# Kernel tuning notes

Hardware: AMD Instinct MI355X
Metric: run time of the kernel (lower is better)

The kernel has to match this reference:

```python
import jax, jax.numpy as jnp
import numpy as np

D = 128      # n_hidden
NC = 4       # n_chan
DEPTH = 2
VD_DEPTH = 1
VD_ATTACH = 0
NV = 100000  # n_verts
PE_LEVELS = 6


def _mlp(x, Ws, bs):
    # MLP: Linear -> ReLU -> Linear -> ReLU -> Linear
    h = jax.nn.relu(x @ Ws[0] + bs[0])
    h = jax.nn.relu(h @ Ws[1] + bs[1])
    return h @ Ws[2] + bs[2]


def setup_inputs() -> dict:
    key = jax.random.key(0)
    ks = jax.random.split(key, 20)
    N, H, W = 2, 512, 512
    inp = {}
    inp["vert_idx_img"] = jax.random.randint(ks[0], (N, H, W, 3), 0, NV, dtype=jnp.int64) if jax.config.read("jax_enable_x64") else jax.random.randint(ks[0], (N, H, W, 3), 0, NV, dtype=jnp.int32)
    inp["bary_img"] = jax.random.uniform(ks[1], (N, H, W, 3), dtype=jnp.float32)
    inp["view_dir"] = jax.random.normal(ks[2], (N, H, W, 3), dtype=jnp.float32)
    # params
    s = D ** (-0.5)
    inp["emb_table"] = jax.random.normal(ks[3], (NV + 1, D), dtype=jnp.float32) * s
    k_lin = np.sqrt(2.0 / D).astype(np.float32)
    inp["vde_W"] = jax.random.normal(ks[4], (3 * PE_LEVELS, D), dtype=jnp.float32) * np.sqrt(2.0 / (3 * PE_LEVELS)).astype(np.float32)
    inp["vde_b"] = jnp.zeros((D,), jnp.float32)
    inp["vh_W"] = jax.random.normal(ks[5], (VD_DEPTH, 3, D, D), dtype=jnp.float32) * k_lin
    inp["vh_b"] = jnp.zeros((VD_DEPTH, 3, D), jnp.float32)
    inp["hid_W"] = jax.random.normal(ks[6], (DEPTH, 3, D, D), dtype=jnp.float32) * k_lin
    inp["hid_b"] = jnp.zeros((DEPTH, 3, D), jnp.float32)
    inp["head_W0"] = jax.random.normal(ks[7], (D, D), dtype=jnp.float32) * k_lin
    inp["head_b0"] = jnp.zeros((D,), jnp.float32)
    inp["head_W1"] = jax.random.normal(ks[8], (D, D), dtype=jnp.float32) * k_lin
    inp["head_b1"] = jnp.zeros((D,), jnp.float32)
    inp["head_W2"] = jax.random.normal(ks[9], (D, NC), dtype=jnp.float32) * k_lin
    inp["head_b2"] = jnp.zeros((NC,), jnp.float32)
    return inp


def reference(vert_idx_img, bary_img, view_dir, emb_table, vde_W, vde_b, vh_W, vh_b,
              hid_W, hid_b, head_W0, head_b0, head_W1, head_b1, head_W2, head_b2):
    # --- embedding gather with max_norm=1.0 renorm (torch nn.Embedding semantics)
    idx = vert_idx_img + 1                       # [N,H,W,3]
    e = emb_table[idx]                           # [N,H,W,3,D]
    nrm = jnp.linalg.norm(e, axis=-1, keepdims=True)
    e = e * jnp.where(nrm > 1.0, 1.0 / (nrm + 1e-7), 1.0)
    # --- barycentric weighted sum over the 3 face vertices
    v = jnp.sum(e * bary_img[..., None], axis=3)  # [N,H,W,D]
    # --- view-direction sin/cos positional encoding (proj_dims=6, val=0.9)
    ll = PE_LEVELS // 2
    exb = 2.0 * jnp.arange(ll, dtype=jnp.float32) / PE_LEVELS
    sigma = 2.0 * jnp.pi / jnp.power(0.9, exb)    # [3]
    pe = view_dir[..., None] * sigma              # [N,H,W,3,3]
    pe = jnp.concatenate([jnp.sin(pe), jnp.cos(pe)], axis=-1)  # [N,H,W,3,6]
    pe = pe.reshape(pe.shape[:-2] + (3 * PE_LEVELS,))           # [N,H,W,18]
    vh = pe @ vde_W + vde_b                       # [N,H,W,D]
    for i in range(vh_W.shape[0]):
        vh = jax.nn.relu(_mlp(vh, vh_W[i], vh_b[i]))
    # --- hidden MLP chain with view-dir modulation at viewdirs_attach
    h = v
    for i in range(hid_W.shape[0]):
        h = jax.nn.relu(_mlp(h, hid_W[i], hid_b[i]))
        if i == VD_ATTACH:
            h = h * vh
    # --- head MLP -> rgba
    rgb = _mlp(h, (head_W0, head_W1, head_W2), (head_b0, head_b1, head_b2))
    return rgb
```

## Files before the change

kernel.cpp:

```cpp
#include <hip/hip_runtime.h>

typedef unsigned int  u32;
typedef unsigned long long u64;
typedef unsigned short u16;
typedef __attribute__((ext_vector_type(8))) _Float16 h8;
typedef __attribute__((ext_vector_type(2))) _Float16 h2;
typedef __attribute__((ext_vector_type(4))) float    f4;

#define RS    136
#define PRS   40
#define PIXB  128
#define WOFF  5120
#define FULLT 16384
#define MFMA16 __builtin_amdgcn_mfma_f32_16x16x32_f16

__device__ __forceinline__ u16 f2h(float f) {
  _Float16 h = (_Float16)f;
  return __builtin_bit_cast(u16, h);
}
__device__ __forceinline__ u32 pkrtz(float a, float b) {
  return __builtin_bit_cast(u32, __builtin_amdgcn_cvt_pkrtz(a, b));
}
__device__ __forceinline__ u32 pkmul(u32 a, u32 b) {
  h2 r = __builtin_bit_cast(h2, a) * __builtin_bit_cast(h2, b);
  return __builtin_bit_cast(u32, r);
}
__device__ __forceinline__ u32 pkmax0(u32 a) {
  h2 z = {(_Float16)0.f, (_Float16)0.f};
  h2 r = __builtin_elementwise_max(__builtin_bit_cast(h2, a), z);
  return __builtin_bit_cast(u32, r);
}

__global__ __launch_bounds__(256) void rc_prep(
    const float* __restrict__ vde_W, const float* __restrict__ vh_W,
    const float* __restrict__ hid_W, const float* __restrict__ head_W0,
    const float* __restrict__ head_W1, const float* __restrict__ head_W2,
    u16* __restrict__ ws)
{
  const int TOT = WOFF + 12 * FULLT;
  int i = blockIdx.x * 256 + threadIdx.x;
  if (i >= TOT) return;
  float val = 0.f;
  if (i < WOFF) {
    int n = i / PRS, k = i - n * PRS;
    if (k < 18) val = vde_W[k * 128 + n];
  } else {
    int t  = i - WOFF;
    int j  = t >> 14;
    int c  = t & 16383;
    int nt = c >> 11;
    int ks = (c >> 9) & 3;
    int ln = (c >> 3) & 63;
    int e  = c & 7;
    int r  = ln & 15, g = ln >> 4;
    int n  = nt * 16 + r;
    int k  = ks * 32 + g * 8 + e;
    if (j < 3)        val = vh_W[j * 16384 + k * 128 + n];
    else if (j < 9)   val = hid_W[(j - 3) * 16384 + k * 128 + n];
    else if (j == 9)  val = head_W0[k * 128 + n];
    else if (j == 10) val = head_W1[k * 128 + n];
    else              val = (n < 4) ? head_W2[k * 4 + n] : 0.f;
  }
  ws[i] = f2h(val);
}

#define GLOAD(dst, base, voff, immstr)                                        \
  asm volatile("global_load_dwordx4 %0, %1, %2 offset:" immstr               \
               : "=v"(dst) : "v"(voff), "s"(base) : "memory")

#define ISSUE(S, NTL) do {                                                    \
  u32 vo_ = aoff + (NTL) * 4096;                                              \
  GLOAD(Ar##S[0], wbase, vo_, "0");                                           \
  GLOAD(Ar##S[1], wbase, vo_, "1024");                                        \
  GLOAD(Ar##S[2], wbase, vo_, "2048");                                        \
  GLOAD(Ar##S[3], wbase, vo_, "3072");                                        \
} while (0)

#define WAITV(nstr) do {                                                      \
  asm volatile("s_waitcnt vmcnt(" nstr ")" ::: "memory");                     \
  __builtin_amdgcn_sched_barrier(0);                                          \
} while (0)

#define COMPUTE_NT(NTL, AA, XNB) do {                                         \
  f4 bini = *(const f4*)&BL[blb + nbase + (NTL) * 16 + 4 * g];                \
  f4 ac[2] = {bini, bini};                                                    \
  _Pragma("unroll")                                                           \
  for (int ks = 0; ks < 4; ++ks) {                                            \
    ac[0] = MFMA16(AA[ks], x[0][ks], ac[0], 0, 0, 0);                         \
    ac[1] = MFMA16(AA[ks], x[1][ks], ac[1], 0, 0, 0);                         \
  }                                                                           \
  const int col = nbase + (NTL) * 16 + 4 * g;                                 \
  _Pragma("unroll")                                                           \
  for (int t = 0; t < 2; ++t) {                                               \
    u32 lo = pkmax0(pkrtz(ac[t][0], ac[t][1]));                               \
    u32 hi = pkmax0(pkrtz(ac[t][2], ac[t][3]));                               \
    if (mode == 1) {                                 \
      vhp[t][NTL][0] = lo; vhp[t][NTL][1] = hi;                               \
    } else {                                                                  \
      if (mode == 2) {                                \
        lo = pkmul(lo, vhp[t][NTL][0]);                                       \
        hi = pkmul(hi, vhp[t][NTL][1]);                                       \
      }                                                                       \
      *(uint2*)&XNB[xr[t] + col] = make_uint2(lo, hi);                        \
    }                                                                         \
  }                                                                           \
} while (0)

#define LAYER(LI, XC, XN) do {                                                \
  const int li   = (LI);                                                      \
  const int blb  = (li + 1) * 128;                                            \
  const int mode = (li == 2) ? 1 : (li == 5) ? 2 : 0;                         \
  const u64 wbase = (u64)(uintptr_t)(ws + WOFF + li * FULLT);                 \
  ISSUE(0, 0); ISSUE(1, 1); ISSUE(2, 2);              \
  h8 x[2][4];                                                                 \
  _Pragma("unroll")                                                           \
  for (int t = 0; t < 2; ++t)                                                 \
    _Pragma("unroll")                                                         \
    for (int ks = 0; ks < 4; ++ks)                                            \
      x[t][ks] = *(const h8*)&XC[xr[t] + ks * 32 + g * 8];                    \
  WAITV("8");  COMPUTE_NT(0, Ar0, XN);  ISSUE(0, 3);                          \
  WAITV("8");  COMPUTE_NT(1, Ar1, XN);                                        \
  WAITV("4");  COMPUTE_NT(2, Ar2, XN);                                        \
  WAITV("0");  COMPUTE_NT(3, Ar0, XN);        \
  if (li == 2) do_gather(XN);                                                 \
  __syncthreads();                             \
} while (0)

__global__ __launch_bounds__(512, 4) void rc_main(
    const int*   __restrict__ vert,  const float* __restrict__ bary,
    const float* __restrict__ view,  const float* __restrict__ emb,
    const float* __restrict__ vde_b, const float* __restrict__ vh_b,
    const float* __restrict__ hid_b, const float* __restrict__ head_b0,
    const float* __restrict__ head_b1, const float* __restrict__ head_b2,
    const u16*   __restrict__ ws,    float* __restrict__ out)
{
  __shared__ __align__(16) u16   X0[PIXB * RS];
  __shared__ __align__(16) u16   X1[PIXB * RS];
  __shared__ __align__(16) float BL[1664];

  const int tid  = threadIdx.x;
  const int lane = tid & 63;
  const int w    = tid >> 6;
  const int pg   = w >> 1;
  const int cg   = w & 1;
  const int r    = lane & 15;
  const int g    = lane >> 4;
  const int pbase = pg * 32;
  const int nbase = cg * 64;
  const u32 aoff  = (u32)(cg * 16384 + lane * 16);
  const size_t bpix = (size_t)blockIdx.x * PIXB;

  for (int i = tid; i < 1664; i += 512) {
    float v;
    if      (i < 128)  v = vde_b[i];
    else if (i < 512)  v = vh_b[i - 128];
    else if (i < 1280) v = hid_b[i - 512];
    else if (i < 1408) v = head_b0[i - 1280];
    else if (i < 1536) v = head_b1[i - 1408];
    else if (i < 1540) v = head_b2[i - 1536];
    else               v = 0.f;
    BL[i] = v;
  }

  if (tid < PIXB) {
    const int p = tid;
    const float* vd = view + (bpix + p) * 3;
    const float SG0 = 6.28318530718f;
    const float SG1 = 6.50777324f;
    const float SG2 = 6.74038866f;
    u32 pw[16];
#pragma unroll
    for (int i = 0; i < 3; ++i) {
      float x = vd[i];
      float s0 = __sinf(x * SG0), c0 = __cosf(x * SG0);
      float s1 = __sinf(x * SG1), c1 = __cosf(x * SG1);
      float s2 = __sinf(x * SG2), c2 = __cosf(x * SG2);
      pw[i * 3 + 0] = (u32)f2h(s0) | ((u32)f2h(s1) << 16);
      pw[i * 3 + 1] = (u32)f2h(s2) | ((u32)f2h(c0) << 16);
      pw[i * 3 + 2] = (u32)f2h(c1) | ((u32)f2h(c2) << 16);
    }
#pragma unroll
    for (int q = 9; q < 16; ++q) pw[q] = 0u;
    uint4* dst = (uint4*)&X0[p * RS];
#pragma unroll
    for (int q = 0; q < 4; ++q)
      dst[q] = make_uint4(pw[4*q], pw[4*q+1], pw[4*q+2], pw[4*q+3]);
  }
  __syncthreads();

  const int xr[2] = { (pbase + r) * RS, (pbase + 16 + r) * RS };

  auto do_gather = [&](u16* XNB) {
#pragma unroll 4
    for (int i = 0; i < 4; ++i) {
      int p = w * 16 + g * 4 + i;
      size_t gp = bpix + p;
      const int*   vi = vert + gp * 3;
      const float* by = bary + gp * 3;
      f4 va = {0.f,0.f,0.f,0.f}, vb = {0.f,0.f,0.f,0.f};
#pragma unroll
      for (int vt = 0; vt < 3; ++vt) {
        int id = vi[vt] + 1;
        const float* row = emb + (size_t)id * 128 + r * 8;
        f4 e0 = *(const f4*)row;
        f4 e1 = *(const f4*)(row + 4);
        float ss = e0[0]*e0[0] + e0[1]*e0[1] + e0[2]*e0[2] + e0[3]*e0[3]
                 + e1[0]*e1[0] + e1[1]*e1[1] + e1[2]*e1[2] + e1[3]*e1[3];
        ss += __shfl_xor(ss, 1);
        ss += __shfl_xor(ss, 2);
        ss += __shfl_xor(ss, 4);
        ss += __shfl_xor(ss, 8);
        float nrm = sqrtf(ss);
        float sc  = (nrm > 1.f) ? (1.f / (nrm + 1e-7f)) : 1.f;
        float wt  = by[vt] * sc;
#pragma unroll
        for (int j = 0; j < 4; ++j) { va[j] += wt * e0[j]; vb[j] += wt * e1[j]; }
      }
      h8 o;
#pragma unroll
      for (int j = 0; j < 4; ++j) { o[j] = (_Float16)va[j]; o[j+4] = (_Float16)vb[j]; }
      *(h8*)&XNB[p * RS + r * 8] = o;
    }
  };

  {
    h8 Av[4];
#pragma unroll
    for (int ntl = 0; ntl < 4; ++ntl)
      Av[ntl] = *(const h8*)&ws[(nbase + ntl * 16 + r) * PRS + g * 8];
    h8 pe[2];
#pragma unroll
    for (int t = 0; t < 2; ++t) pe[t] = *(const h8*)&X0[xr[t] + g * 8];
#pragma unroll
    for (int ntl = 0; ntl < 4; ++ntl) {
      f4 bini = *(const f4*)&BL[nbase + ntl * 16 + 4 * g];
      const int col = nbase + ntl * 16 + 4 * g;
#pragma unroll
      for (int t = 0; t < 2; ++t) {
        f4 acc = MFMA16(Av[ntl], pe[t], bini, 0, 0, 0);
        *(uint2*)&X1[xr[t] + col] =
          make_uint2(pkrtz(acc[0], acc[1]), pkrtz(acc[2], acc[3]));
      }
    }
  }
  __syncthreads();

  u32 vhp[2][4][2];
  h8 Ar0[4], Ar1[4], Ar2[4];
  LAYER(0, X1, X0);  LAYER(1, X0, X1);
  LAYER(2, X1, X0);  LAYER(3, X0, X1);
  LAYER(4, X1, X0);  LAYER(5, X0, X1);
  LAYER(6, X1, X0);  LAYER(7, X0, X1);
  LAYER(8, X1, X0);  LAYER(9, X0, X1);
  LAYER(10, X1, X0);

  if (cg == 0) {
    h8 x[2][4];
#pragma unroll
    for (int t = 0; t < 2; ++t)
#pragma unroll
      for (int ks = 0; ks < 4; ++ks)
        x[t][ks] = *(const h8*)&X0[xr[t] + ks * 32 + g * 8];
    const u16* wa = ws + WOFF + 11 * FULLT;
    f4 b2 = *(const f4*)&BL[1536 + 4 * g];
    f4 acc[2] = {b2, b2};
#pragma unroll
    for (int ks = 0; ks < 4; ++ks) {
      h8 A = *(const h8*)&wa[ks * 512 + lane * 8];
#pragma unroll
      for (int t = 0; t < 2; ++t)
        acc[t] = MFMA16(A, x[t][ks], acc[t], 0, 0, 0);
    }
    if (g == 0) {
#pragma unroll
      for (int t = 0; t < 2; ++t)
        *(f4*)&out[(bpix + pbase + t * 16 + r) * 4] = acc[t];
    }
  }
}

extern "C" void kernel_launch(void* const* d_in, const int* in_sizes, int n_in,
                              void* d_out, int out_size, void* d_ws, size_t ws_size,
                              hipStream_t stream) {
  const int*   vert    = (const int*)  d_in[0];
  const float* bary    = (const float*)d_in[1];
  const float* view    = (const float*)d_in[2];
  const float* emb     = (const float*)d_in[3];
  const float* vde_W   = (const float*)d_in[4];
  const float* vde_b   = (const float*)d_in[5];
  const float* vh_W    = (const float*)d_in[6];
  const float* vh_b    = (const float*)d_in[7];
  const float* hid_W   = (const float*)d_in[8];
  const float* hid_b   = (const float*)d_in[9];
  const float* head_W0 = (const float*)d_in[10];
  const float* head_b0 = (const float*)d_in[11];
  const float* head_W1 = (const float*)d_in[12];
  const float* head_b1 = (const float*)d_in[13];
  const float* head_W2 = (const float*)d_in[14];
  const float* head_b2 = (const float*)d_in[15];
  u16* wsp = (u16*)d_ws;

  rc_prep<<<788, 256, 0, stream>>>(vde_W, vh_W, hid_W, head_W0, head_W1, head_W2, wsp);
  rc_main<<<4096, 512, 0, stream>>>(vert, bary, view, emb, vde_b, vh_b, hid_b,
                                    head_b0, head_b1, head_b2, wsp, (float*)d_out);
}
```

Baseline: 312.4 us.

## Retile MLP warps to 64 pixels by 32 columns per wave

```diff
diff --git a/kernel.cpp b/kernel.cpp
--- a/kernel.cpp
+++ b/kernel.cpp
@@ -81,17 +81,23 @@
   __builtin_amdgcn_sched_barrier(0);                                          \
 } while (0)
 
-#define COMPUTE_NT(NTL, AA, XNB) do {                                         \
+#define COMPUTE_NT(NTL, AA, XC, XNB) do {                                     \
   f4 bini = *(const f4*)&BL[blb + nbase + (NTL) * 16 + 4 * g];                \
-  f4 ac[2] = {bini, bini};                                                    \
+  f4 ac[4] = {bini, bini, bini, bini};                                        \
   _Pragma("unroll")                                                           \
   for (int ks = 0; ks < 4; ++ks) {                                            \
-    ac[0] = MFMA16(AA[ks], x[0][ks], ac[0], 0, 0, 0);                         \
-    ac[1] = MFMA16(AA[ks], x[1][ks], ac[1], 0, 0, 0);                         \
+    h8 x0_ = *(const h8*)&XC[xr[0] + ks * 32 + g * 8];                        \
+    h8 x1_ = *(const h8*)&XC[xr[1] + ks * 32 + g * 8];                        \
+    h8 x2_ = *(const h8*)&XC[xr[2] + ks * 32 + g * 8];                        \
+    h8 x3_ = *(const h8*)&XC[xr[3] + ks * 32 + g * 8];                        \
+    ac[0] = MFMA16(AA[ks], x0_, ac[0], 0, 0, 0);                              \
+    ac[1] = MFMA16(AA[ks], x1_, ac[1], 0, 0, 0);                              \
+    ac[2] = MFMA16(AA[ks], x2_, ac[2], 0, 0, 0);                              \
+    ac[3] = MFMA16(AA[ks], x3_, ac[3], 0, 0, 0);                              \
   }                                                                           \
   const int col = nbase + (NTL) * 16 + 4 * g;                                 \
   _Pragma("unroll")                                                           \
-  for (int t = 0; t < 2; ++t) {                                               \
+  for (int t = 0; t < 4; ++t) {                                               \
     u32 lo = pkmax0(pkrtz(ac[t][0], ac[t][1]));                               \
     u32 hi = pkmax0(pkrtz(ac[t][2], ac[t][3]));                               \
     if (mode == 1) {                                 \
@@ -111,17 +117,9 @@
   const int blb  = (li + 1) * 128;                                            \
   const int mode = (li == 2) ? 1 : (li == 5) ? 2 : 0;                         \
   const u64 wbase = (u64)(uintptr_t)(ws + WOFF + li * FULLT);                 \
-  ISSUE(0, 0); ISSUE(1, 1); ISSUE(2, 2);              \
-  h8 x[2][4];                                                                 \
-  _Pragma("unroll")                                                           \
-  for (int t = 0; t < 2; ++t)                                                 \
-    _Pragma("unroll")                                                         \
-    for (int ks = 0; ks < 4; ++ks)                                            \
-      x[t][ks] = *(const h8*)&XC[xr[t] + ks * 32 + g * 8];                    \
-  WAITV("8");  COMPUTE_NT(0, Ar0, XN);  ISSUE(0, 3);                          \
-  WAITV("8");  COMPUTE_NT(1, Ar1, XN);                                        \
-  WAITV("4");  COMPUTE_NT(2, Ar2, XN);                                        \
-  WAITV("0");  COMPUTE_NT(3, Ar0, XN);        \
+  ISSUE(0, 0); ISSUE(1, 1);                            \
+  WAITV("4");  COMPUTE_NT(0, Ar0, XC, XN);                                    \
+  WAITV("0");  COMPUTE_NT(1, Ar1, XC, XN);         \
   if (li == 2) do_gather(XN);                                                 \
   __syncthreads();                             \
 } while (0)
@@ -141,13 +139,13 @@
   const int tid  = threadIdx.x;
   const int lane = tid & 63;
   const int w    = tid >> 6;
-  const int pg   = w >> 1;
-  const int cg   = w & 1;
+  const int pg   = w >> 2;
+  const int cq   = w & 3;
   const int r    = lane & 15;
   const int g    = lane >> 4;
-  const int pbase = pg * 32;
-  const int nbase = cg * 64;
-  const u32 aoff  = (u32)(cg * 16384 + lane * 16);
+  const int pbase = pg * 64;
+  const int nbase = cq * 32;
+  const u32 aoff  = (u32)(cq * 8192 + lane * 16);
   const size_t bpix = (size_t)blockIdx.x * PIXB;
 
   for (int i = tid; i < 1664; i += 512) {
@@ -188,7 +186,8 @@
   }
   __syncthreads();
 
-  const int xr[2] = { (pbase + r) * RS, (pbase + 16 + r) * RS };
+  const int xr[4] = { (pbase +      r) * RS, (pbase + 16 + r) * RS,
+                      (pbase + 32 + r) * RS, (pbase + 48 + r) * RS };
 
   auto do_gather = [&](u16* XNB) {
 #pragma unroll 4
@@ -224,19 +223,19 @@
   };
 
   {
-    h8 Av[4];
-#pragma unroll
-    for (int ntl = 0; ntl < 4; ++ntl)
+    h8 Av[2];
+#pragma unroll
+    for (int ntl = 0; ntl < 2; ++ntl)
       Av[ntl] = *(const h8*)&ws[(nbase + ntl * 16 + r) * PRS + g * 8];
-    h8 pe[2];
-#pragma unroll
-    for (int t = 0; t < 2; ++t) pe[t] = *(const h8*)&X0[xr[t] + g * 8];
-#pragma unroll
-    for (int ntl = 0; ntl < 4; ++ntl) {
+    h8 pe[4];
+#pragma unroll
+    for (int t = 0; t < 4; ++t) pe[t] = *(const h8*)&X0[xr[t] + g * 8];
+#pragma unroll
+    for (int ntl = 0; ntl < 2; ++ntl) {
       f4 bini = *(const f4*)&BL[nbase + ntl * 16 + 4 * g];
       const int col = nbase + ntl * 16 + 4 * g;
 #pragma unroll
-      for (int t = 0; t < 2; ++t) {
+      for (int t = 0; t < 4; ++t) {
         f4 acc = MFMA16(Av[ntl], pe[t], bini, 0, 0, 0);
         *(uint2*)&X1[xr[t] + col] =
           make_uint2(pkrtz(acc[0], acc[1]), pkrtz(acc[2], acc[3]));
@@ -245,8 +244,8 @@
   }
   __syncthreads();
 
-  u32 vhp[2][4][2];
-  h8 Ar0[4], Ar1[4], Ar2[4];
+  u32 vhp[4][2][2];
+  h8 Ar0[4], Ar1[4];
   LAYER(0, X1, X0);  LAYER(1, X0, X1);
   LAYER(2, X1, X0);  LAYER(3, X0, X1);
   LAYER(4, X1, X0);  LAYER(5, X0, X1);
@@ -254,26 +253,22 @@
   LAYER(8, X1, X0);  LAYER(9, X0, X1);
   LAYER(10, X1, X0);
 
-  if (cg == 0) {
-    h8 x[2][4];
-#pragma unroll
-    for (int t = 0; t < 2; ++t)
-#pragma unroll
-      for (int ks = 0; ks < 4; ++ks)
-        x[t][ks] = *(const h8*)&X0[xr[t] + ks * 32 + g * 8];
+  if (cq == 0) {
     const u16* wa = ws + WOFF + 11 * FULLT;
     f4 b2 = *(const f4*)&BL[1536 + 4 * g];
-    f4 acc[2] = {b2, b2};
+    f4 acc[4] = {b2, b2, b2, b2};
 #pragma unroll
     for (int ks = 0; ks < 4; ++ks) {
       h8 A = *(const h8*)&wa[ks * 512 + lane * 8];
 #pragma unroll
-      for (int t = 0; t < 2; ++t)
-        acc[t] = MFMA16(A, x[t][ks], acc[t], 0, 0, 0);
+      for (int t = 0; t < 4; ++t) {
+        h8 xt = *(const h8*)&X0[xr[t] + ks * 32 + g * 8];
+        acc[t] = MFMA16(A, xt, acc[t], 0, 0, 0);
+      }
     }
     if (g == 0) {
 #pragma unroll
-      for (int t = 0; t < 2; ++t)
+      for (int t = 0; t < 4; ++t)
         *(f4*)&out[(bpix + pbase + t * 16 + r) * 4] = acc[t];
     }
   }
```

Measured after the change: 322.0 us. +3.1%, slower.
